# Kernel tuning notes

Hardware: AMD Instinct MI355X
Metric: run time of the kernel (lower is better)

## Reference

```python
import jax, jax.numpy as jnp
import numpy as np

C = 0.01          # Poincare ball curvature 1/100
SQRT_C = 0.1
EPS = 1e-15
BALL_EPS = 4e-3   # geoopt float32 projx boundary epsilon


def _norm(x):
    return jnp.linalg.norm(x, axis=-1, keepdims=True)


def expmap0(u):
    n = jnp.maximum(_norm(u), EPS)
    return jnp.tanh(SQRT_C * n) * u / (SQRT_C * n)


def logmap0(x):
    n = jnp.maximum(_norm(x), EPS)
    t = jnp.clip(SQRT_C * n, -1.0 + 1e-7, 1.0 - 1e-7)
    return jnp.arctanh(t) * x / (SQRT_C * n)


def projx(x):
    maxnorm = (1.0 - BALL_EPS) / SQRT_C
    n = jnp.maximum(_norm(x), EPS)
    return jnp.where(n > maxnorm, x / n * maxnorm, x)


def mobius_matvec(M, x):
    xn = jnp.maximum(_norm(x), EPS)
    mx = x @ M.T
    mxn = jnp.maximum(_norm(mx), EPS)
    t = jnp.clip(SQRT_C * xn, -1.0 + 1e-7, 1.0 - 1e-7)
    res = jnp.tanh(mxn / xn * jnp.arctanh(t)) * mx / (mxn * SQRT_C)
    return jnp.where(jnp.all(mx == 0, axis=-1, keepdims=True), 0.0, res)


def mobius_add(x, y):
    x2 = jnp.sum(x * x, -1, keepdims=True)
    y2 = jnp.sum(y * y, -1, keepdims=True)
    xy = jnp.sum(x * y, -1, keepdims=True)
    num = (1 + 2 * C * xy + C * y2) * x + (1 - C * x2) * y
    den = 1 + 2 * C * xy + C * C * x2 * y2
    return num / jnp.maximum(den, EPS)


def hyp_linear(x, W, b):
    # eval mode: weight dropout is a no-op
    res = projx(mobius_matvec(W, x))
    hb = projx(expmap0(b.reshape(1, -1)))
    return projx(mobius_add(res, hb))


def setup_inputs() -> dict:
    key = jax.random.key(0)
    ks = jax.random.split(key, 10)
    B, S, N, H, HEADS, E = 2, 4, 10000, 64, 4, 160000
    G = B * S
    OC = H // HEADS
    # edges guaranteed to have no self-loops (module removes then re-adds them)
    src = jax.random.randint(ks[0], (G, E), 0, N)
    off = jax.random.randint(ks[1], (G, E), 1, N)
    dst = (src + off) % N
    edge_index = jnp.stack([src, dst], axis=1).astype(jnp.int32)  # [G,2,E]

    def glorot(k, shape, fan):
        a = np.sqrt(6.0 / fan)
        return jax.random.uniform(k, shape, minval=-a, maxval=a, dtype=jnp.float32)

    emb = jax.random.normal(ks[2], (N, H), dtype=jnp.float32)
    att_i = glorot(ks[3], (1, HEADS, OC), HEADS * OC + 1)
    att_j = glorot(ks[4], (1, HEADS, OC), HEADS * OC + 1)
    w1 = glorot(ks[5], (H, OC), H + OC)   # HypLinear(in=16, out=64): weight [out,in]
    b1 = jnp.zeros((H,), jnp.float32)
    w2 = glorot(ks[6], (H, H), H + H)
    b2 = jnp.zeros((H,), jnp.float32)
    history_graphs = jnp.zeros((B, S, N), jnp.float32)  # only shape is used
    return {"history_graphs": history_graphs, "edge_index": edge_index,
            "emb": emb, "att_i": att_i, "att_j": att_j,
            "w1": w1, "b1": b1, "w2": w2, "b2": b2}


def reference(history_graphs, edge_index, emb, att_i, att_j, w1, b1, w2, b2):
    B, S, N = history_graphs.shape
    G = edge_index.shape[0]
    H = emb.shape[1]
    heads = att_i.shape[1]
    oc = H // heads

    # node ids are arange(N) for every (b,s) -> identical features per graph
    x0 = projx(expmap0(emb))   # initHyperX, [N,H]
    xt = logmap0(x0)           # tangent features used by attention, [N,H]

    # add self loops (inputs contain none)
    loops = jnp.broadcast_to(jnp.arange(N, dtype=edge_index.dtype)[None, None, :], (G, 2, N))
    ei = jnp.concatenate([edge_index, loops], axis=-1)  # [G,2,E+N]

    def agg(e):
        src, dst = e[0], e[1]                       # targets (i), sources (j)
        x_i = xt[src].reshape(-1, heads, oc)        # [E2,h,oc]
        x_j = xt[dst].reshape(-1, heads, oc)
        alpha = jnp.sum(x_i * att_i, -1) + jnp.sum(x_j * att_j, -1)  # [E2,h]
        alpha = jax.nn.leaky_relu(alpha, 0.2)
        m = jax.ops.segment_max(alpha, src, num_segments=N)
        a = jnp.exp(alpha - m[src])
        s = jax.ops.segment_sum(a, src, num_segments=N)
        a = a / (s[src] + 1e-16)                    # edge softmax; dropout eval no-op
        sup = jax.ops.segment_sum(x_j * a[..., None], src, num_segments=N)  # [N,h,oc]
        sup = sup.mean(axis=1)                      # concat=False -> head mean, [N,oc]
        return projx(expmap0(sup))

    h = jax.vmap(agg)(ei)                           # [G,N,oc]
    node_emb = h.reshape(B, S, N, oc)[:, -1]        # last timestep, [B,N,oc]

    z = hyp_linear(node_emb, w1, b1)                # 16 -> 64
    z = projx(expmap0(jax.nn.silu(logmap0(z))))     # HypAct(SiLU)
    z = projx(expmap0(logmap0(z)))                  # HypDropout (eval: log/exp round trip)
    z = hyp_linear(z, w2, b2)                       # 64 -> 64
    return z
```

## Files before the change

### kernel.cpp

```cpp
#include <hip/hip_runtime.h>
#include <hip/hip_bf16.h>

#define N_NODES 10000
#define NE 160000
#define CAP 96
#define SQRT_C 0.1f
#define RINV_SQRT_C 10.0f
#define CC 0.01f
#define EPS 1e-15f
#define MAXNORM ((1.0f - 4e-3f) / SQRT_C)
#define RMAXNORM (1.0f / MAXNORM)

__device__ __forceinline__ float frcp(float x) { return __builtin_amdgcn_rcpf(x); }
__device__ __forceinline__ float frsq(float x) { return __builtin_amdgcn_rsqf(x); }

__device__ __forceinline__ float fexp(float x) { return __expf(x); }
__device__ __forceinline__ float ftanh_pos(float x) {
    return 1.0f - 2.0f * frcp(__expf(2.0f * x) + 1.0f);
}
__device__ __forceinline__ float fatanh01(float t) {
    return 0.5f * __logf((1.0f + t) * frcp(1.0f - t));
}

__device__ __forceinline__ float ldf(const void* p, int i, int isbf) {
    return isbf ? __bfloat162float(((const __hip_bfloat16*)p)[i])
                : ((const float*)p)[i];
}

__device__ __forceinline__ int sniff_wave(const void* emb, int tid) {
    unsigned wv = ((const unsigned*)emb)[tid & 63];
    unsigned ex = (wv >> 7) & 0xFFu;
    unsigned long long m = __ballot(ex >= 116u && ex <= 133u);
    return (__popcll(m) >= 32) ? 1 : 0;
}

__device__ __forceinline__ float wsum(float v) {
#pragma unroll
    for (int off = 32; off > 0; off >>= 1) v += __shfl_xor(v, off, 64);
    return v;
}
__device__ __forceinline__ float wmax(float v) {
#pragma unroll
    for (int off = 32; off > 0; off >>= 1) v = fmaxf(v, __shfl_xor(v, off, 64));
    return v;
}

__device__ __forceinline__ float dpp_wsum(float x) {
    int t;
    t = __builtin_amdgcn_update_dpp(0, __float_as_int(x), 0x111, 0xF, 0xF, true);
    x += __int_as_float(t);
    t = __builtin_amdgcn_update_dpp(0, __float_as_int(x), 0x112, 0xF, 0xF, true);
    x += __int_as_float(t);
    t = __builtin_amdgcn_update_dpp(0, __float_as_int(x), 0x114, 0xF, 0xE, true);
    x += __int_as_float(t);
    t = __builtin_amdgcn_update_dpp(0, __float_as_int(x), 0x118, 0xF, 0xC, true);
    x += __int_as_float(t);
    t = __builtin_amdgcn_update_dpp(0, __float_as_int(x), 0x142, 0xA, 0xF, true);
    x += __int_as_float(t);
    t = __builtin_amdgcn_update_dpp(0, __float_as_int(x), 0x143, 0xC, 0xF, true);
    x += __int_as_float(t);
    return __int_as_float(__builtin_amdgcn_readlane(__float_as_int(x), 63));
}

__global__ __launch_bounds__(256) void pre_scatter(const void* __restrict__ emb,
                                                   const void* __restrict__ att_i,
                                                   const void* __restrict__ att_j,
                                                   const void* __restrict__ w1g,
                                                   const void* __restrict__ b1g,
                                                   const void* __restrict__ w2g,
                                                   const void* __restrict__ b2g,
                                                   const int* __restrict__ ei,
                                                   float* __restrict__ xt,
                                                   float* __restrict__ ai,
                                                   float* __restrict__ aj,
                                                   int* __restrict__ cnt,
                                                   unsigned short* __restrict__ bucket,
                                                   int* __restrict__ ovf_cnt,
                                                   unsigned* __restrict__ ovf,
                                                   int* __restrict__ flag,
                                                   float* __restrict__ wf1t,
                                                   float* __restrict__ wf2t,
                                                   float* __restrict__ hb1f,
                                                   float* __restrict__ hb2f,
                                                   float* __restrict__ hbn2) {
    __shared__ int sflag;
    int tid = threadIdx.x;
    int w = tid >> 6, lane = tid & 63;
    if (blockIdx.x < 2500) {
        if (tid < 64) { int s = sniff_wave(emb, tid); if (tid == 0) sflag = s; }
        __syncthreads();
        int isbf = sflag;
        int t = blockIdx.x * 256 + tid;
        int node = t >> 6;
        float u = ldf(emb, node * 64 + lane, isbf);
        float n2c = fmaxf(wsum(u * u), 1e-30f);
        float rn = frsq(n2c);
        float n = n2c * rn;
        float th = ftanh_pos(SQRT_C * n);
        float x0 = th * RINV_SQRT_C * rn * u;
        float x0n = th * RINV_SQRT_C;
        if (x0n > MAXNORM) { x0 *= MAXNORM * frcp(x0n); x0n = MAXNORM; }
        float tc = fminf(SQRT_C * x0n, 1.0f - 1e-7f);
        float xv = fatanh01(tc) * RINV_SQRT_C * frcp(x0n) * x0;
        xt[node * 64 + lane] = xv;
        float pi = xv * ldf(att_i, lane, isbf);
        float pj = xv * ldf(att_j, lane, isbf);
#pragma unroll
        for (int off = 8; off > 0; off >>= 1) {
            pi += __shfl_xor(pi, off, 64);
            pj += __shfl_xor(pj, off, 64);
        }
        if ((lane & 15) == 0) {
            ai[node * 4 + (lane >> 4)] = pi;
            aj[node * 4 + (lane >> 4)] = pj;
        }
    } else if (blockIdx.x < 2813) {
        int e0 = (blockIdx.x - 2500) * 512 + tid;
#pragma unroll
        for (int q = 0; q < 2; ++q) {
            int e = e0 + q * 256;
            if (e >= NE) break;
            int s0 = ei[3 * 2 * NE + e], d0 = ei[3 * 2 * NE + NE + e];
            int s1 = ei[7 * 2 * NE + e], d1 = ei[7 * 2 * NE + NE + e];
            int i0 = s0, i1 = N_NODES + s1;
            int p0 = atomicAdd(&cnt[i0], 1);
            int p1 = atomicAdd(&cnt[i1], 1);
            if (p0 < CAP) bucket[i0 * CAP + p0] = (unsigned short)d0;
            else {
                int oi = atomicAdd(ovf_cnt, 1);
                ovf[oi] = (0u << 28) | ((unsigned)s0 << 14) | (unsigned)d0;
            }
            if (p1 < CAP) bucket[i1 * CAP + p1] = (unsigned short)d1;
            else {
                int oi = atomicAdd(ovf_cnt, 1);
                ovf[oi] = (1u << 28) | ((unsigned)s1 << 14) | (unsigned)d1;
            }
        }
    } else {
        if (tid < 64) { int s = sniff_wave(emb, tid); if (tid == 0) sflag = s; }
        __syncthreads();
        int isbf = sflag;
        if (tid == 0) *flag = isbf;
        for (int i = tid; i < 1024; i += 256) {
            int o = i >> 4, c = i & 15;
            wf1t[c * 64 + o] = ldf(w1g, i, isbf);
        }
        for (int i = tid; i < 4096; i += 256) {
            int o = i >> 6, c = i & 63;
            wf2t[c * 64 + o] = ldf(w2g, i, isbf);
        }
        if (w < 2) {
            const void* bg = w ? b2g : b1g;
            float b = ldf(bg, lane, isbf);
            float n2c = fmaxf(wsum(b * b), 1e-30f);
            float rn = frsq(n2c);
            float n = n2c * rn;
            float th = ftanh_pos(SQRT_C * n);
            float hv = th * RINV_SQRT_C * rn * b;
            float hn = th * RINV_SQRT_C;
            if (hn > MAXNORM) { hv *= MAXNORM * frcp(hn); hn = MAXNORM; }
            (w ? hb2f : hb1f)[lane] = hv;
            if (lane == 0) hbn2[w] = hn * hn;
        }
    }
}

__global__ __launch_bounds__(256) void node_agg(const int* __restrict__ cnt,
                                                const unsigned short* __restrict__ bucket,
                                                const int* __restrict__ ovf_cnt,
                                                const unsigned* __restrict__ ovf,
                                                const float* __restrict__ ai,
                                                const float* __restrict__ aj,
                                                const float* __restrict__ xt,
                                                float* __restrict__ sup_t) {
    __shared__ float wlds[4][64 * 4];
    __shared__ int dlds[4][64];
    int w = threadIdx.x >> 6, lane = threadIdx.x & 63;
    int idx = blockIdx.x * 4 + w;
    int slot = (idx >= N_NODES) ? 1 : 0;
    int n = idx - slot * N_NODES;
    int deg = cnt[idx];
    int start = idx * CAP;

    float4 ai4 = *(const float4*)&ai[n * 4];
    float4 aj4n = *(const float4*)&aj[n * 4];
    float ain[4] = {ai4.x, ai4.y, ai4.z, ai4.w};
    float ajn[4] = {aj4n.x, aj4n.y, aj4n.z, aj4n.w};
    int hh = lane >> 4;
    float acc;

    if (deg <= 63) {
        bool act = (lane <= deg);
        int d = (lane < deg) ? (int)bucket[start + lane] : n;
        float4 a4 = act ? *(const float4*)&aj[d * 4] : make_float4(0.f, 0.f, 0.f, 0.f);
        float ajv[4] = {a4.x, a4.y, a4.z, a4.w};
        float eh[4];
#pragma unroll
        for (int h = 0; h < 4; ++h) {
            float a = ain[h] + ajv[h];
            a = (a < 0.0f) ? 0.2f * a : a;
            eh[h] = act ? fexp(a) : 0.0f;
        }
        float sh[4];
#pragma unroll
        for (int h = 0; h < 4; ++h) sh[h] = wsum(eh[h]);
#pragma unroll
        for (int h = 0; h < 4; ++h)
            wlds[w][lane * 4 + h] = eh[h] * (0.25f * frcp(sh[h] + 1e-16f));
        dlds[w][lane] = d;
        int m = deg + 1;
        float s0 = 0.f, s1 = 0.f, s2 = 0.f, s3 = 0.f;
        float s4 = 0.f, s5 = 0.f, s6 = 0.f, s7 = 0.f;
        int e = 0;
        for (; e + 8 <= m; e += 8) {
            int d0 = dlds[w][e],     d1 = dlds[w][e + 1];
            int d2 = dlds[w][e + 2], d3 = dlds[w][e + 3];
            int d4 = dlds[w][e + 4], d5 = dlds[w][e + 5];
            int d6 = dlds[w][e + 6], d7 = dlds[w][e + 7];
            float w0 = wlds[w][(e + 0) * 4 + hh], w1 = wlds[w][(e + 1) * 4 + hh];
            float w2 = wlds[w][(e + 2) * 4 + hh], w3 = wlds[w][(e + 3) * 4 + hh];
            float w4 = wlds[w][(e + 4) * 4 + hh], w5 = wlds[w][(e + 5) * 4 + hh];
            float w6 = wlds[w][(e + 6) * 4 + hh], w7 = wlds[w][(e + 7) * 4 + hh];
            s0 = fmaf(w0, xt[d0 * 64 + lane], s0);
            s1 = fmaf(w1, xt[d1 * 64 + lane], s1);
            s2 = fmaf(w2, xt[d2 * 64 + lane], s2);
            s3 = fmaf(w3, xt[d3 * 64 + lane], s3);
            s4 = fmaf(w4, xt[d4 * 64 + lane], s4);
            s5 = fmaf(w5, xt[d5 * 64 + lane], s5);
            s6 = fmaf(w6, xt[d6 * 64 + lane], s6);
            s7 = fmaf(w7, xt[d7 * 64 + lane], s7);
        }
        for (; e + 4 <= m; e += 4) {
            int d0 = dlds[w][e],     d1 = dlds[w][e + 1];
            int d2 = dlds[w][e + 2], d3 = dlds[w][e + 3];
            float w0 = wlds[w][(e + 0) * 4 + hh], w1 = wlds[w][(e + 1) * 4 + hh];
            float w2 = wlds[w][(e + 2) * 4 + hh], w3 = wlds[w][(e + 3) * 4 + hh];
            s0 = fmaf(w0, xt[d0 * 64 + lane], s0);
            s1 = fmaf(w1, xt[d1 * 64 + lane], s1);
            s2 = fmaf(w2, xt[d2 * 64 + lane], s2);
            s3 = fmaf(w3, xt[d3 * 64 + lane], s3);
        }
        for (; e < m; ++e)
            s0 = fmaf(wlds[w][e * 4 + hh], xt[dlds[w][e] * 64 + lane], s0);
        acc = ((s0 + s1) + (s2 + s3)) + ((s4 + s5) + (s6 + s7));
    } else {
        int bdeg = (deg < CAP) ? deg : CAP;
        int tov = (deg > CAP) ? *ovf_cnt : 0;
        float mh[4];
#pragma unroll
        for (int h = 0; h < 4; ++h) {
            float a = ain[h] + ajn[h];
            mh[h] = (a < 0.0f) ? 0.2f * a : a;
        }
        for (int e = lane; e < bdeg; e += 64) {
            int d = bucket[start + e];
#pragma unroll
            for (int h = 0; h < 4; ++h) {
                float a = ain[h] + aj[d * 4 + h];
                a = (a < 0.0f) ? 0.2f * a : a;
                mh[h] = fmaxf(mh[h], a);
            }
        }
        for (int k = lane; k < tov; k += 64) {
            unsigned pe = ovf[k];
            if ((int)(pe >> 28) == slot && (int)((pe >> 14) & 0x3FFFu) == n) {
                int d = pe & 0x3FFFu;
#pragma unroll
                for (int h = 0; h < 4; ++h) {
                    float a = ain[h] + aj[d * 4 + h];
                    a = (a < 0.0f) ? 0.2f * a : a;
                    mh[h] = fmaxf(mh[h], a);
                }
            }
        }
#pragma unroll
        for (int h = 0; h < 4; ++h) mh[h] = wmax(mh[h]);
        float sh[4] = {0.f, 0.f, 0.f, 0.f};
        if (lane == 0) {
#pragma unroll
            for (int h = 0; h < 4; ++h) {
                float a = ain[h] + ajn[h];
                a = (a < 0.0f) ? 0.2f * a : a;
                sh[h] = fexp(a - mh[h]);
            }
        }
        for (int e = lane; e < bdeg; e += 64) {
            int d = bucket[start + e];
#pragma unroll
            for (int h = 0; h < 4; ++h) {
                float a = ain[h] + aj[d * 4 + h];
                a = (a < 0.0f) ? 0.2f * a : a;
                sh[h] += fexp(a - mh[h]);
            }
        }
        for (int k = lane; k < tov; k += 64) {
            unsigned pe = ovf[k];
            if ((int)(pe >> 28) == slot && (int)((pe >> 14) & 0x3FFFu) == n) {
                int d = pe & 0x3FFFu;
#pragma unroll
                for (int h = 0; h < 4; ++h) {
                    float a = ain[h] + aj[d * 4 + h];
                    a = (a < 0.0f) ? 0.2f * a : a;
                    sh[h] += fexp(a - mh[h]);
                }
            }
        }
#pragma unroll
        for (int h = 0; h < 4; ++h) sh[h] = wsum(sh[h]);
        float scale[4];
#pragma unroll
        for (int h = 0; h < 4; ++h) scale[h] = 0.25f * frcp(sh[h] + 1e-16f);
        float aih = ain[hh], mhh = mh[hh], sch = scale[hh];
        float aself = aih + ajn[hh];
        aself = (aself < 0.0f) ? 0.2f * aself : aself;
        acc = fexp(aself - mhh) * sch * xt[n * 64 + lane];
        for (int e = 0; e < bdeg; ++e) {
            int d = bucket[start + e];
            float a = aih + aj[d * 4 + hh];
            a = (a < 0.0f) ? 0.2f * a : a;
            acc = fmaf(fexp(a - mhh) * sch, xt[d * 64 + lane], acc);
        }
        for (int k = 0; k < tov; ++k) {
            unsigned pe = ovf[k];
            if ((int)(pe >> 28) == slot && (int)((pe >> 14) & 0x3FFFu) == n) {
                int d = pe & 0x3FFFu;
                float a = aih + aj[d * 4 + hh];
                a = (a < 0.0f) ? 0.2f * a : a;
                acc = fmaf(fexp(a - mhh) * sch, xt[d * 64 + lane], acc);
            }
        }
    }
    acc += __shfl_xor(acc, 16, 64);
    acc += __shfl_xor(acc, 32, 64);
    if (lane < 16) sup_t[idx * 16 + lane] = acc;
}

__global__ __launch_bounds__(256) void final_stage(const float* __restrict__ sup_t,
                                                   const float* __restrict__ wf1t,
                                                   const float* __restrict__ wf2t,
                                                   const float* __restrict__ hb1f,
                                                   const float* __restrict__ hb2f,
                                                   const float* __restrict__ hbn2,
                                                   const int* __restrict__ flag,
                                                   void* __restrict__ outv) {
    __shared__ float vz[4][80];
    int tid = threadIdx.x, w = tid >> 6, lane = tid & 63;
    float w2r[64];
#pragma unroll
    for (int c = 0; c < 64; ++c) w2r[c] = wf2t[c * 64 + lane];
    float w1r[16];
#pragma unroll
    for (int c = 0; c < 16; ++c) w1r[c] = wf1t[c * 64 + lane];
    float hb1 = hb1f[lane], hb2v = hb2f[lane];
    float y2a = hbn2[0], y2b = hbn2[1];
    int isbf = *flag;
    float* vbuf = vz[w];
    float* zbuf = vz[w] + 16;
    int nb = (blockIdx.x * 4 + w) * 4;

    float vls[4];
#pragma unroll
    for (int k = 0; k < 4; ++k)
        vls[k] = (lane < 16) ? sup_t[(nb + k) * 16 + lane] : 0.0f;

#pragma unroll 1
    for (int k = 0; k < 4; ++k) {
        float vl = vls[k];
        if (lane < 16) vbuf[lane] = vl;
        float n2c = fmaxf(dpp_wsum(vl * vl), 1e-30f);
        float rnv = frsq(n2c);
        float n = n2c * rnv;
        float th0 = ftanh_pos(SQRT_C * n);
        float s0 = th0 * RINV_SQRT_C * rnv;
        float x0n = th0 * RINV_SQRT_C;
        if (x0n > MAXNORM) { s0 *= MAXNORM * frcp(x0n); x0n = MAXNORM; }

        float a1 = 0.f;
#pragma unroll
        for (int j = 0; j < 4; ++j) {
            const float4 vq = *(const float4*)&vbuf[j * 4];
            a1 = fmaf(w1r[4 * j + 0], vq.x, a1);
            a1 = fmaf(w1r[4 * j + 1], vq.y, a1);
            a1 = fmaf(w1r[4 * j + 2], vq.z, a1);
            a1 = fmaf(w1r[4 * j + 3], vq.w, a1);
        }
        a1 *= s0;

        float mxn2 = dpp_wsum(a1 * a1);
        float mxhb = dpp_wsum(a1 * hb1);
        float xn = fmaxf(x0n, EPS);
        float mxc = fmaxf(mxn2, 1e-30f);
        float rmx = frsq(mxc);
        float mxn = mxc * rmx;
        float t = fminf(SQRT_C * xn, 1.0f - 1e-7f);
        float th = ftanh_pos(mxn * frcp(xn) * fatanh01(t));
        float rs = th * RINV_SQRT_C * rmx;
        float rn = th * RINV_SQRT_C;
        if (mxn2 == 0.0f) { rs = 0.f; rn = 0.f; }
        if (rn > MAXNORM) { rs *= MAXNORM * frcp(rn); rn = MAXNORM; }
        float xy = rs * mxhb;
        float x2 = rn * rn;
        float A = 1.0f + 2.0f * CC * xy + CC * y2a;
        float B = 1.0f - CC * x2;
        float rden = frcp(fmaxf(1.0f + 2.0f * CC * xy + CC * CC * x2 * y2a, EPS));
        float z = (A * rs * a1 + B * hb1) * rden;

        float znc = fmaxf(dpp_wsum(z * z), 1e-30f);
        float rzn = frsq(znc);
        float zn = znc * rzn;
        float sc = (zn > MAXNORM) ? MAXNORM * rzn : 1.0f;
        float z1n = fminf(zn, MAXNORM);
        float rz1n = (zn > MAXNORM) ? RMAXNORM : rzn;
        float lg = fatanh01(fminf(SQRT_C * z1n, 1.0f - 1e-7f)) * RINV_SQRT_C * rz1n * sc;
        float u = lg * z;
        u = u * frcp(1.0f + __expf(-u));

        float unc = fmaxf(dpp_wsum(u * u), 1e-30f);
        float run = frsq(unc);
        float un = unc * run;
        float th2 = ftanh_pos(SQRT_C * un);
        float s2 = th2 * RINV_SQRT_C * run;
        float z2n = th2 * RINV_SQRT_C;
        if (z2n > MAXNORM) { s2 *= MAXNORM * frcp(z2n); z2n = MAXNORM; }
        float z2 = u * s2;

        zbuf[lane] = z2;
        float a2 = 0.f;
#pragma unroll
        for (int j = 0; j < 16; ++j) {
            const float4 zq = *(const float4*)&zbuf[j * 4];
            a2 = fmaf(w2r[4 * j + 0], zq.x, a2);
            a2 = fmaf(w2r[4 * j + 1], zq.y, a2);
            a2 = fmaf(w2r[4 * j + 2], zq.z, a2);
            a2 = fmaf(w2r[4 * j + 3], zq.w, a2);
        }

        float pn2 = dpp_wsum(a2 * a2);
        float ph2 = dpp_wsum(a2 * hb2v);
        float xnb = fmaxf(z2n, EPS);
        float pnc = fmaxf(pn2, 1e-30f);
        float rpx = frsq(pnc);
        float mxnb = pnc * rpx;
        float tb = fminf(SQRT_C * xnb, 1.0f - 1e-7f);
        float thb = ftanh_pos(mxnb * frcp(xnb) * fatanh01(tb));
        float rsb = thb * RINV_SQRT_C * rpx;
        float rnb = thb * RINV_SQRT_C;
        if (pn2 == 0.0f) { rsb = 0.f; rnb = 0.f; }
        if (rnb > MAXNORM) { rsb *= MAXNORM * frcp(rnb); rnb = MAXNORM; }
        float xyb = rsb * ph2;
        float x2b = rnb * rnb;
        float Ab = 1.0f + 2.0f * CC * xyb + CC * y2b;
        float Bb = 1.0f - CC * x2b;
        float rdenb = frcp(fmaxf(1.0f + 2.0f * CC * xyb + CC * CC * x2b * y2b, EPS));
        float zf = (Ab * rsb * a2 + Bb * hb2v) * rdenb;
        float zfc = fmaxf(dpp_wsum(zf * zf), 1e-30f);
        float rzf = frsq(zfc);
        float znf = zfc * rzf;
        float s4 = (znf > MAXNORM) ? MAXNORM * rzf : 1.0f;
        float val = zf * s4;

        if (isbf) ((__hip_bfloat16*)outv)[(nb + k) * 64 + lane] = __float2bfloat16(val);
        else      ((float*)outv)[(nb + k) * 64 + lane] = val;
    }
}

extern "C" void kernel_launch(void* const* d_in, const int* in_sizes, int n_in,
                              void* d_out, int out_size, void* d_ws, size_t ws_size,
                              hipStream_t stream) {
    const int* ei = (const int*)d_in[1];
    const void* emb   = d_in[2];
    const void* att_i = d_in[3];
    const void* att_j = d_in[4];
    const void* w1 = d_in[5];
    const void* b1 = d_in[6];
    const void* w2 = d_in[7];
    const void* b2 = d_in[8];

    float* ws = (float*)d_ws;
    float* xt    = ws;
    float* ai    = ws + 640000;
    float* aj    = ws + 680000;
    float* sup_t = ws + 720000;
    int* cnt     = (int*)(ws + 1040000);
    int* ovf_cnt = (int*)(ws + 1060000);
    unsigned short* bucket = (unsigned short*)(ws + 1060032);
    unsigned* ovf = (unsigned*)(ws + 2020032);
    int* flag     = (int*)(ws + 2340032);
    float* wf1t = ws + 2340064;
    float* wf2t = ws + 2341088;
    float* hb1f = ws + 2345184;
    float* hb2f = ws + 2345248;
    float* hbn2 = ws + 2345312;

    hipMemsetAsync((void*)cnt, 0, (2 * N_NODES + 8) * sizeof(int), stream);
    hipLaunchKernelGGL(pre_scatter, dim3(2814), dim3(256), 0, stream,
                       emb, att_i, att_j, w1, b1, w2, b2, ei,
                       xt, ai, aj, cnt, bucket, ovf_cnt, ovf, flag,
                       wf1t, wf2t, hb1f, hb2f, hbn2);
    hipLaunchKernelGGL(node_agg, dim3(5000), dim3(256), 0, stream,
                       cnt, bucket, ovf_cnt, ovf, ai, aj, xt, sup_t);
    hipLaunchKernelGGL(final_stage, dim3(1250), dim3(256), 0, stream,
                       sup_t, wf1t, wf2t, hb1f, hb2f, hbn2, flag, d_out);
}
```

Baseline: 137.0 us.

## Fuse hyperbolic head stage into node aggregation kernel

Merges the final HypLinear/HypAct/HypLinear stage into the per-node aggregation kernel, so each wave computes its node's output directly from the aggregated accumulator. This removes a kernel launch and the sup_t write and re-read through global memory. Because every lane now holds the replicated aggregate, the squared-norm reduction is scaled by 0.25 to compensate. In exchange, the weight matrices are read from global/cache per wave instead of being kept in registers and amortized over four nodes. The added code may also raise register pressure in the gather-heavy aggregation kernel and lower its occupancy.

```diff
diff --git a/kernel.cpp b/kernel.cpp
--- a/kernel.cpp
+++ b/kernel.cpp
@@ -165,14 +165,20 @@
     }
 }
 
-__global__ __launch_bounds__(256) void node_agg(const int* __restrict__ cnt,
+__global__ __launch_bounds__(256) void agg_head(const int* __restrict__ cnt,
                                                 const unsigned short* __restrict__ bucket,
                                                 const int* __restrict__ ovf_cnt,
                                                 const unsigned* __restrict__ ovf,
                                                 const float* __restrict__ ai,
                                                 const float* __restrict__ aj,
                                                 const float* __restrict__ xt,
-                                                float* __restrict__ sup_t) {
+                                                const float* __restrict__ wf1t,
+                                                const float* __restrict__ wf2t,
+                                                const float* __restrict__ hb1f,
+                                                const float* __restrict__ hb2f,
+                                                const float* __restrict__ hbn2,
+                                                const int* __restrict__ flag,
+                                                void* __restrict__ outv) {
     __shared__ float wlds[4][64 * 4];
     __shared__ int dlds[4][64];
     int w = threadIdx.x >> 6, lane = threadIdx.x & 63;
@@ -332,136 +338,109 @@
     }
     acc += __shfl_xor(acc, 16, 64);
     acc += __shfl_xor(acc, 32, 64);
-    if (lane < 16) sup_t[idx * 16 + lane] = acc;
-}
-
-__global__ __launch_bounds__(256) void final_stage(const float* __restrict__ sup_t,
-                                                   const float* __restrict__ wf1t,
-                                                   const float* __restrict__ wf2t,
-                                                   const float* __restrict__ hb1f,
-                                                   const float* __restrict__ hb2f,
-                                                   const float* __restrict__ hbn2,
-                                                   const int* __restrict__ flag,
-                                                   void* __restrict__ outv) {
-    __shared__ float vz[4][80];
-    int tid = threadIdx.x, w = tid >> 6, lane = tid & 63;
-    float w2r[64];
-#pragma unroll
-    for (int c = 0; c < 64; ++c) w2r[c] = wf2t[c * 64 + lane];
-    float w1r[16];
-#pragma unroll
-    for (int c = 0; c < 16; ++c) w1r[c] = wf1t[c * 64 + lane];
+
+    float vl = acc;
+    float* vbuf = wlds[w];
+    float* zbuf = wlds[w] + 16;
+    if (lane < 16) vbuf[lane] = vl;
+    int isbf = *flag;
+    float y2a = hbn2[0], y2b = hbn2[1];
     float hb1 = hb1f[lane], hb2v = hb2f[lane];
-    float y2a = hbn2[0], y2b = hbn2[1];
-    int isbf = *flag;
-    float* vbuf = vz[w];
-    float* zbuf = vz[w] + 16;
-    int nb = (blockIdx.x * 4 + w) * 4;
-
-    float vls[4];
-#pragma unroll
-    for (int k = 0; k < 4; ++k)
-        vls[k] = (lane < 16) ? sup_t[(nb + k) * 16 + lane] : 0.0f;
-
-#pragma unroll 1
-    for (int k = 0; k < 4; ++k) {
-        float vl = vls[k];
-        if (lane < 16) vbuf[lane] = vl;
-        float n2c = fmaxf(dpp_wsum(vl * vl), 1e-30f);
-        float rnv = frsq(n2c);
-        float n = n2c * rnv;
-        float th0 = ftanh_pos(SQRT_C * n);
-        float s0 = th0 * RINV_SQRT_C * rnv;
-        float x0n = th0 * RINV_SQRT_C;
-        if (x0n > MAXNORM) { s0 *= MAXNORM * frcp(x0n); x0n = MAXNORM; }
-
-        float a1 = 0.f;
-#pragma unroll
-        for (int j = 0; j < 4; ++j) {
-            const float4 vq = *(const float4*)&vbuf[j * 4];
-            a1 = fmaf(w1r[4 * j + 0], vq.x, a1);
-            a1 = fmaf(w1r[4 * j + 1], vq.y, a1);
-            a1 = fmaf(w1r[4 * j + 2], vq.z, a1);
-            a1 = fmaf(w1r[4 * j + 3], vq.w, a1);
-        }
-        a1 *= s0;
-
-        float mxn2 = dpp_wsum(a1 * a1);
-        float mxhb = dpp_wsum(a1 * hb1);
-        float xn = fmaxf(x0n, EPS);
-        float mxc = fmaxf(mxn2, 1e-30f);
-        float rmx = frsq(mxc);
-        float mxn = mxc * rmx;
-        float t = fminf(SQRT_C * xn, 1.0f - 1e-7f);
-        float th = ftanh_pos(mxn * frcp(xn) * fatanh01(t));
-        float rs = th * RINV_SQRT_C * rmx;
-        float rn = th * RINV_SQRT_C;
-        if (mxn2 == 0.0f) { rs = 0.f; rn = 0.f; }
-        if (rn > MAXNORM) { rs *= MAXNORM * frcp(rn); rn = MAXNORM; }
-        float xy = rs * mxhb;
-        float x2 = rn * rn;
-        float A = 1.0f + 2.0f * CC * xy + CC * y2a;
-        float B = 1.0f - CC * x2;
-        float rden = frcp(fmaxf(1.0f + 2.0f * CC * xy + CC * CC * x2 * y2a, EPS));
-        float z = (A * rs * a1 + B * hb1) * rden;
-
-        float znc = fmaxf(dpp_wsum(z * z), 1e-30f);
-        float rzn = frsq(znc);
-        float zn = znc * rzn;
-        float sc = (zn > MAXNORM) ? MAXNORM * rzn : 1.0f;
-        float z1n = fminf(zn, MAXNORM);
-        float rz1n = (zn > MAXNORM) ? RMAXNORM : rzn;
-        float lg = fatanh01(fminf(SQRT_C * z1n, 1.0f - 1e-7f)) * RINV_SQRT_C * rz1n * sc;
-        float u = lg * z;
-        u = u * frcp(1.0f + __expf(-u));
-
-        float unc = fmaxf(dpp_wsum(u * u), 1e-30f);
-        float run = frsq(unc);
-        float un = unc * run;
-        float th2 = ftanh_pos(SQRT_C * un);
-        float s2 = th2 * RINV_SQRT_C * run;
-        float z2n = th2 * RINV_SQRT_C;
-        if (z2n > MAXNORM) { s2 *= MAXNORM * frcp(z2n); z2n = MAXNORM; }
-        float z2 = u * s2;
-
-        zbuf[lane] = z2;
-        float a2 = 0.f;
-#pragma unroll
-        for (int j = 0; j < 16; ++j) {
-            const float4 zq = *(const float4*)&zbuf[j * 4];
-            a2 = fmaf(w2r[4 * j + 0], zq.x, a2);
-            a2 = fmaf(w2r[4 * j + 1], zq.y, a2);
-            a2 = fmaf(w2r[4 * j + 2], zq.z, a2);
-            a2 = fmaf(w2r[4 * j + 3], zq.w, a2);
-        }
-
-        float pn2 = dpp_wsum(a2 * a2);
-        float ph2 = dpp_wsum(a2 * hb2v);
-        float xnb = fmaxf(z2n, EPS);
-        float pnc = fmaxf(pn2, 1e-30f);
-        float rpx = frsq(pnc);
-        float mxnb = pnc * rpx;
-        float tb = fminf(SQRT_C * xnb, 1.0f - 1e-7f);
-        float thb = ftanh_pos(mxnb * frcp(xnb) * fatanh01(tb));
-        float rsb = thb * RINV_SQRT_C * rpx;
-        float rnb = thb * RINV_SQRT_C;
-        if (pn2 == 0.0f) { rsb = 0.f; rnb = 0.f; }
-        if (rnb > MAXNORM) { rsb *= MAXNORM * frcp(rnb); rnb = MAXNORM; }
-        float xyb = rsb * ph2;
-        float x2b = rnb * rnb;
-        float Ab = 1.0f + 2.0f * CC * xyb + CC * y2b;
-        float Bb = 1.0f - CC * x2b;
-        float rdenb = frcp(fmaxf(1.0f + 2.0f * CC * xyb + CC * CC * x2b * y2b, EPS));
-        float zf = (Ab * rsb * a2 + Bb * hb2v) * rdenb;
-        float zfc = fmaxf(dpp_wsum(zf * zf), 1e-30f);
-        float rzf = frsq(zfc);
-        float znf = zfc * rzf;
-        float s4 = (znf > MAXNORM) ? MAXNORM * rzf : 1.0f;
-        float val = zf * s4;
-
-        if (isbf) ((__hip_bfloat16*)outv)[(nb + k) * 64 + lane] = __float2bfloat16(val);
-        else      ((float*)outv)[(nb + k) * 64 + lane] = val;
+
+    float n2c = fmaxf(0.25f * dpp_wsum(vl * vl), 1e-30f);
+    float rnv = frsq(n2c);
+    float nn = n2c * rnv;
+    float th0 = ftanh_pos(SQRT_C * nn);
+    float s0v = th0 * RINV_SQRT_C * rnv;
+    float x0n = th0 * RINV_SQRT_C;
+    if (x0n > MAXNORM) { s0v *= MAXNORM * frcp(x0n); x0n = MAXNORM; }
+
+    float a1 = 0.f;
+#pragma unroll
+    for (int j = 0; j < 4; ++j) {
+        const float4 vq = *(const float4*)&vbuf[j * 4];
+        a1 = fmaf(wf1t[(4 * j + 0) * 64 + lane], vq.x, a1);
+        a1 = fmaf(wf1t[(4 * j + 1) * 64 + lane], vq.y, a1);
+        a1 = fmaf(wf1t[(4 * j + 2) * 64 + lane], vq.z, a1);
+        a1 = fmaf(wf1t[(4 * j + 3) * 64 + lane], vq.w, a1);
     }
+    a1 *= s0v;
+
+    float mxn2 = dpp_wsum(a1 * a1);
+    float mxhb = dpp_wsum(a1 * hb1);
+    float xn = fmaxf(x0n, EPS);
+    float mxc = fmaxf(mxn2, 1e-30f);
+    float rmx = frsq(mxc);
+    float mxn = mxc * rmx;
+    float t = fminf(SQRT_C * xn, 1.0f - 1e-7f);
+    float th = ftanh_pos(mxn * frcp(xn) * fatanh01(t));
+    float rs = th * RINV_SQRT_C * rmx;
+    float rn = th * RINV_SQRT_C;
+    if (mxn2 == 0.0f) { rs = 0.f; rn = 0.f; }
+    if (rn > MAXNORM) { rs *= MAXNORM * frcp(rn); rn = MAXNORM; }
+    float xy = rs * mxhb;
+    float x2 = rn * rn;
+    float A = 1.0f + 2.0f * CC * xy + CC * y2a;
+    float B = 1.0f - CC * x2;
+    float rden = frcp(fmaxf(1.0f + 2.0f * CC * xy + CC * CC * x2 * y2a, EPS));
+    float z = (A * rs * a1 + B * hb1) * rden;
+
+    float znc = fmaxf(dpp_wsum(z * z), 1e-30f);
+    float rzn = frsq(znc);
+    float zn = znc * rzn;
+    float scz = (zn > MAXNORM) ? MAXNORM * rzn : 1.0f;
+    float z1n = fminf(zn, MAXNORM);
+    float rz1n = (zn > MAXNORM) ? RMAXNORM : rzn;
+    float lg = fatanh01(fminf(SQRT_C * z1n, 1.0f - 1e-7f)) * RINV_SQRT_C * rz1n * scz;
+    float u = lg * z;
+    u = u * frcp(1.0f + __expf(-u));
+
+    float unc = fmaxf(dpp_wsum(u * u), 1e-30f);
+    float run = frsq(unc);
+    float un = unc * run;
+    float th2 = ftanh_pos(SQRT_C * un);
+    float s2 = th2 * RINV_SQRT_C * run;
+    float z2n = th2 * RINV_SQRT_C;
+    if (z2n > MAXNORM) { s2 *= MAXNORM * frcp(z2n); z2n = MAXNORM; }
+    float z2 = u * s2;
+
+    zbuf[lane] = z2;
+    float a2 = 0.f;
+#pragma unroll
+    for (int j = 0; j < 16; ++j) {
+        const float4 zq = *(const float4*)&zbuf[j * 4];
+        a2 = fmaf(wf2t[(4 * j + 0) * 64 + lane], zq.x, a2);
+        a2 = fmaf(wf2t[(4 * j + 1) * 64 + lane], zq.y, a2);
+        a2 = fmaf(wf2t[(4 * j + 2) * 64 + lane], zq.z, a2);
+        a2 = fmaf(wf2t[(4 * j + 3) * 64 + lane], zq.w, a2);
+    }
+
+    float pn2 = dpp_wsum(a2 * a2);
+    float ph2 = dpp_wsum(a2 * hb2v);
+    float xnb = fmaxf(z2n, EPS);
+    float pnc = fmaxf(pn2, 1e-30f);
+    float rpx = frsq(pnc);
+    float mxnb = pnc * rpx;
+    float tb = fminf(SQRT_C * xnb, 1.0f - 1e-7f);
+    float thb = ftanh_pos(mxnb * frcp(xnb) * fatanh01(tb));
+    float rsb = thb * RINV_SQRT_C * rpx;
+    float rnb = thb * RINV_SQRT_C;
+    if (pn2 == 0.0f) { rsb = 0.f; rnb = 0.f; }
+    if (rnb > MAXNORM) { rsb *= MAXNORM * frcp(rnb); rnb = MAXNORM; }
+    float xyb = rsb * ph2;
+    float x2b = rnb * rnb;
+    float Ab = 1.0f + 2.0f * CC * xyb + CC * y2b;
+    float Bb = 1.0f - CC * x2b;
+    float rdenb = frcp(fmaxf(1.0f + 2.0f * CC * xyb + CC * CC * x2b * y2b, EPS));
+    float zf = (Ab * rsb * a2 + Bb * hb2v) * rdenb;
+    float zfc = fmaxf(dpp_wsum(zf * zf), 1e-30f);
+    float rzf = frsq(zfc);
+    float znf = zfc * rzf;
+    float s4 = (znf > MAXNORM) ? MAXNORM * rzf : 1.0f;
+    float val = zf * s4;
+
+    if (isbf) ((__hip_bfloat16*)outv)[idx * 64 + lane] = __float2bfloat16(val);
+    else      ((float*)outv)[idx * 64 + lane] = val;
 }
 
 extern "C" void kernel_launch(void* const* d_in, const int* in_sizes, int n_in,
@@ -480,7 +459,6 @@
     float* xt    = ws;
     float* ai    = ws + 640000;
     float* aj    = ws + 680000;
-    float* sup_t = ws + 720000;
     int* cnt     = (int*)(ws + 1040000);
     int* ovf_cnt = (int*)(ws + 1060000);
     unsigned short* bucket = (unsigned short*)(ws + 1060032);
@@ -497,8 +475,7 @@
                        emb, att_i, att_j, w1, b1, w2, b2, ei,
                        xt, ai, aj, cnt, bucket, ovf_cnt, ovf, flag,
                        wf1t, wf2t, hb1f, hb2f, hbn2);
-    hipLaunchKernelGGL(node_agg, dim3(5000), dim3(256), 0, stream,
-                       cnt, bucket, ovf_cnt, ovf, ai, aj, xt, sup_t);
-    hipLaunchKernelGGL(final_stage, dim3(1250), dim3(256), 0, stream,
-                       sup_t, wf1t, wf2t, hb1f, hb2f, hbn2, flag, d_out);
-}
+    hipLaunchKernelGGL(agg_head, dim3(5000), dim3(256), 0, stream,
+                       cnt, bucket, ovf_cnt, ovf, ai, aj, xt,
+                       wf1t, wf2t, hb1f, hb2f, hbn2, flag, d_out);
+}
```

Result: faster. 129.4 us (median of 2 runs) (-5.5%).
